# Optimization experiments

Measured on AMD Instinct MI355X. Metric: run time of the kernel, lower is better.

Reference implementation:

```python
import jax, jax.numpy as jnp
import numpy as np

E = 8            # num experts
D = 1024         # hidden size
F = 4096         # ffn hidden size
CAP_FACTOR = 2.0 # expert-choice capacity factor


def setup_inputs() -> dict:
    key = jax.random.key(0)
    ks = jax.random.split(key, 6)
    B, S = 8, 1024
    hidden_states = jax.random.normal(ks[0], (B, S, D), dtype=jnp.float32)
    Wg = jax.random.normal(ks[1], (D, E), dtype=jnp.float32) * (1.0 / np.sqrt(D))
    W1 = jax.random.normal(ks[2], (E, D, F), dtype=jnp.float32) * (1.0 / np.sqrt(D))
    b1 = jnp.zeros((E, F), dtype=jnp.float32)
    W2 = jax.random.normal(ks[3], (E, F, D), dtype=jnp.float32) * (1.0 / np.sqrt(F))
    b2 = jnp.zeros((E, D), dtype=jnp.float32)
    return {"hidden_states": hidden_states, "Wg": Wg, "W1": W1, "b1": b1,
            "W2": W2, "b2": b2}


def reference(hidden_states, Wg, W1, b1, W2, b2):
    B, S, d = hidden_states.shape
    T = B * S
    C = int(T * CAP_FACTOR / E)  # capacity per expert (static)

    x = hidden_states.reshape(T, d)                      # [T, D]
    gates = jax.nn.softmax(x @ Wg, axis=-1)              # [T, E] router probs

    # Expert-choice routing: each expert picks its top-C tokens.
    scores = gates.T                                     # [E, T]
    top_vals, idx = jax.lax.top_k(scores, C)             # [E, C]

    # Load-balancing aux loss (mean gate prob * fraction routed, per expert).
    frac_routed = jnp.zeros((T, E), gates.dtype).at[
        idx.reshape(-1), jnp.repeat(jnp.arange(E), C)].set(1.0).mean(axis=0)
    aux_loss = E * jnp.sum(gates.mean(axis=0) * frac_routed)

    # Grouped expert FFN on gathered tokens.
    xg = x[idx]                                          # [E, C, D]
    h = jax.nn.gelu(jnp.einsum('ecd,edf->ecf', xg, W1) + b1[:, None, :])
    yo = jnp.einsum('ecf,efd->ecd', h, W2) + b2[:, None, :]  # [E, C, D]

    # Weight by routing prob and scatter-add back to token positions.
    weighted = yo * top_vals[..., None]                  # [E, C, D]
    out = jnp.zeros((T, d), x.dtype).at[idx.reshape(-1)].add(
        weighted.reshape(-1, d))
    return out.reshape(B, S, d), aux_loss
```

## Files before the change

### kernel.cpp

```cpp
#include <hip/hip_runtime.h>
#include <hip/hip_bf16.h>

#define T_TOK 8192
#define E_EXP 8
#define D_HID 1024
#define F_FFN 4096
#define C_CAP 2048

typedef __attribute__((ext_vector_type(8))) short bf16x8;
typedef __attribute__((ext_vector_type(4))) float f32x4;

__device__ __forceinline__ void load_lds16(const void* g, void* l) {
    __builtin_amdgcn_global_load_lds(
        (const __attribute__((address_space(1))) unsigned int*)g,
        (__attribute__((address_space(3))) unsigned int*)l, 16, 0, 0);
}

__device__ __forceinline__ float gelu_fast(float v) {
    float z = v * (1.5957691216057308f + 0.07135481627f * v * v);
    return v / (1.0f + __expf(-z));
}

__global__ __launch_bounds__(256) void gating_kernel(
    const float* __restrict__ x, const float* __restrict__ Wg,
    float* __restrict__ gatesT, __hip_bfloat16* __restrict__ xbf,
    float* __restrict__ aux_out)
{
    const int token = blockIdx.x * 4 + (threadIdx.x >> 6);
    const int lane  = threadIdx.x & 63;
    if (token == 0 && lane == 0)
        aux_out[0] = (float)E_EXP * (float)C_CAP / (float)T_TOK;
    const float* xr = x + (size_t)token * D_HID;

    float acc[E_EXP];
#pragma unroll
    for (int e = 0; e < E_EXP; ++e) acc[e] = 0.0f;

#pragma unroll
    for (int it = 0; it < 4; ++it) {
        const int c4 = it * 64 + lane;
        float4 v = ((const float4*)xr)[c4];
        float vv[4] = {v.x, v.y, v.z, v.w};
        union { __hip_bfloat16 h[4]; short4 s; } u;
#pragma unroll
        for (int j = 0; j < 4; ++j) u.h[j] = __float2bfloat16(vv[j]);
        ((short4*)(xbf + (size_t)token * D_HID))[c4] = u.s;
        const float* wr0 = Wg + (size_t)c4 * 4 * E_EXP;
#pragma unroll
        for (int j = 0; j < 4; ++j)
#pragma unroll
            for (int e = 0; e < E_EXP; ++e) acc[e] += vv[j] * wr0[j * E_EXP + e];
    }
#pragma unroll
    for (int e = 0; e < E_EXP; ++e) {
        for (int off = 32; off; off >>= 1) acc[e] += __shfl_down(acc[e], off);
    }
    if (lane == 0) {
        float m = acc[0];
#pragma unroll
        for (int e = 1; e < E_EXP; ++e) m = fmaxf(m, acc[e]);
        float ex[E_EXP];
        float s = 0.0f;
#pragma unroll
        for (int e = 0; e < E_EXP; ++e) { ex[e] = expf(acc[e] - m); s += ex[e]; }
        float inv = 1.0f / s;
#pragma unroll
        for (int e = 0; e < E_EXP; ++e) gatesT[(size_t)e * T_TOK + token] = ex[e] * inv;
    }
}

__global__ __launch_bounds__(1024) void topk_kernel(
    const float* __restrict__ gatesT, int* __restrict__ topidx,
    float* __restrict__ topval, int* __restrict__ cnt, int* __restrict__ inv)
{
    __shared__ unsigned long long keys[T_TOK];
    __shared__ unsigned long long sel[C_CAP];
    __shared__ unsigned int hist[256];
    __shared__ unsigned int cum[256];
    __shared__ unsigned int bc_v, bc_r;
    __shared__ unsigned int selcnt;

    const int e   = blockIdx.x;
    const int tid = threadIdx.x;
    const float* row = gatesT + (size_t)e * T_TOK;

    for (int i = tid; i < T_TOK; i += 1024) {
        unsigned int b = __float_as_uint(row[i]);
        b = (b & 0x80000000u) ? ~b : (b | 0x80000000u);
        keys[i] = ((unsigned long long)b << 32) | (unsigned int)(T_TOK - 1 - i);
    }
    if (tid == 0) selcnt = 0;
    __syncthreads();

    unsigned long long prefix = 0ull, mask = 0ull;
    unsigned int rank = C_CAP;
    for (int byte = 7; byte >= 0; --byte) {
        if (tid < 256) hist[tid] = 0;
        __syncthreads();
        const int sh = byte * 8;
        for (int i = tid; i < T_TOK; i += 1024) {
            unsigned long long k = keys[i];
            if ((k & mask) == prefix)
                atomicAdd(&hist[(unsigned int)((k >> sh) & 255ull)], 1u);
        }
        __syncthreads();
        if (tid < 256) cum[tid] = hist[tid];
        __syncthreads();
        for (int off = 1; off < 256; off <<= 1) {
            unsigned int add = 0;
            if (tid < 256 && tid + off < 256) add = cum[tid + off];
            __syncthreads();
            if (tid < 256) cum[tid] += add;
            __syncthreads();
        }
        if (tid < 256) {
            unsigned int ge = cum[tid];
            unsigned int gt = (tid < 255) ? cum[tid + 1] : 0u;
            if (ge >= rank && gt < rank) { bc_v = (unsigned int)tid; bc_r = rank - gt; }
        }
        __syncthreads();
        prefix |= ((unsigned long long)bc_v) << sh;
        mask   |= (0xFFull << sh);
        rank = bc_r;
        __syncthreads();
    }
    const unsigned long long thr = prefix;

    for (int i = tid; i < T_TOK; i += 1024) {
        unsigned long long k = keys[i];
        if (k >= thr) sel[atomicAdd(&selcnt, 1u)] = k;
    }
    __syncthreads();

    for (int k = 2; k <= C_CAP; k <<= 1) {
        for (int j = k >> 1; j > 0; j >>= 1) {
            for (int i = tid; i < C_CAP; i += 1024) {
                int p = i ^ j;
                if (p > i) {
                    bool desc = ((i & k) == 0);
                    unsigned long long a = sel[i];
                    unsigned long long b = sel[p];
                    bool sw = desc ? (a < b) : (a > b);
                    if (sw) { sel[i] = b; sel[p] = a; }
                }
            }
            __syncthreads();
        }
    }

    for (int c = tid; c < C_CAP; c += 1024) {
        unsigned long long kk = sel[c];
        int idx = T_TOK - 1 - (int)(kk & 0xFFFFFFFFu);
        unsigned int b = (unsigned int)(kk >> 32);
        b = (b & 0x80000000u) ? (b & 0x7FFFFFFFu) : ~b;
        topidx[e * C_CAP + c] = idx;
        topval[e * C_CAP + c] = __uint_as_float(b);
        int slot = atomicAdd(&cnt[idx], 1);
        inv[idx * E_EXP + slot] = e * C_CAP + c;
    }
}

__global__ __launch_bounds__(256) void transpose_bf16_kernel(
    const float* __restrict__ in, __hip_bfloat16* __restrict__ out,
    int R, int Cn)
{
    __shared__ float tile[64][65];
    const int e = blockIdx.z;
    in  += (size_t)e * R * Cn;
    out += (size_t)e * R * Cn;
    const int c0 = blockIdx.x * 64, r0 = blockIdx.y * 64;
    const int tid = threadIdx.x;

    const int lr = tid >> 4, lc4 = (tid & 15) * 4;
#pragma unroll
    for (int it = 0; it < 4; ++it) {
        int r = lr + it * 16;
        float4 v = *(const float4*)(in + (size_t)(r0 + r) * Cn + c0 + lc4);
        tile[r][lc4 + 0] = v.x; tile[r][lc4 + 1] = v.y;
        tile[r][lc4 + 2] = v.z; tile[r][lc4 + 3] = v.w;
    }
    __syncthreads();

    const int ocb = tid >> 3, j0 = (tid & 7) * 8;
#pragma unroll
    for (int it = 0; it < 2; ++it) {
        int oc = ocb + it * 32;
        union { __hip_bfloat16 h[8]; uint4 v; } u;
#pragma unroll
        for (int j = 0; j < 8; ++j) u.h[j] = __float2bfloat16(tile[j0 + j][oc]);
        *(uint4*)(out + (size_t)(c0 + oc) * R + r0 + j0) = u.v;
    }
}


#define BARS do { __builtin_amdgcn_s_barrier(); __builtin_amdgcn_sched_barrier(0); } while (0)
#define WLG  do { asm volatile("s_waitcnt lgkmcnt(0)" ::: "memory"); __builtin_amdgcn_sched_barrier(0); } while (0)
#define VMC4 asm volatile("s_waitcnt vmcnt(4)" ::: "memory")
#define VMC0 asm volatile("s_waitcnt vmcnt(0)" ::: "memory")

#define G_STAGE_A(hh, s) do { int b_ = (((s) & 1) << 15) + ((hh) << 14) + (w << 10); \
    load_lds16(Abase + (size_t)(aog[hh][0] + (s) * 128), smem + b_); \
    load_lds16(Abase + (size_t)(aog[hh][1] + (s) * 128), smem + b_ + 8192); } while (0)
#define G_STAGE_B(hh, s) do { int b_ = 65536 + (((s) & 1) << 15) + ((hh) << 14) + (w << 10); \
    load_lds16(Bbase + (size_t)(bog[hh][0] + (s) * 128), smem + b_); \
    load_lds16(Bbase + (size_t)(bog[hh][1] + (s) * 128), smem + b_ + 8192); } while (0)

#define READ_A(mh) do { _Pragma("unroll") for (int mi = 0; mi < 4; ++mi) { \
    aF[mi][0] = *(const bf16x8*)(Ab + (arow + (mh) * 8192 + mi * 2048 + kc0)); \
    aF[mi][1] = *(const bf16x8*)(Ab + (arow + (mh) * 8192 + mi * 2048 + kc1)); } } while (0)
#define READ_B(nh, dst) do { _Pragma("unroll") for (int ni = 0; ni < 2; ++ni) { \
    dst[ni][0] = *(const bf16x8*)(Bb + (brow + (nh) * 4096 + ni * 2048 + kc0)); \
    dst[ni][1] = *(const bf16x8*)(Bb + (brow + (nh) * 4096 + ni * 2048 + kc1)); } } while (0)

#define QUAD(mh, nh, BF) do { \
    __builtin_amdgcn_s_setprio(1); \
    _Pragma("unroll") for (int mi = 0; mi < 4; ++mi) \
    _Pragma("unroll") for (int ni = 0; ni < 2; ++ni) { \
        acc[(mh)*4+mi][(nh)*2+ni] = __builtin_amdgcn_mfma_f32_16x16x32_bf16( \
            aF[mi][0], BF[ni][0], acc[(mh)*4+mi][(nh)*2+ni], 0, 0, 0); \
        acc[(mh)*4+mi][(nh)*2+ni] = __builtin_amdgcn_mfma_f32_16x16x32_bf16( \
            aF[mi][1], BF[ni][1], acc[(mh)*4+mi][(nh)*2+ni], 0, 0, 0); } \
    __builtin_amdgcn_s_setprio(0); } while (0)

#define GEMM_PROLOGUE() do { \
    G_STAGE_A(0, 0); G_STAGE_A(1, 0); G_STAGE_B(0, 0); G_STAGE_B(1, 0); \
    G_STAGE_B(0, 1); G_STAGE_B(1, 1); \
    VMC4; BARS; } while (0)

#define GEMM_TILE(t, NT) do { \
    const char* Ab = smem + (((t) & 1) << 15); \
    const char* Bb = smem + 65536 + (((t) & 1) << 15); \
     \
    READ_A(0); READ_B(0, bF0); \
    if ((t) + 1 < (NT)) G_STAGE_A(0, (t) + 1); \
    BARS; WLG; QUAD(0, 0, bF0); BARS; \
     \
    READ_B(1, bF1); \
    if ((t) + 1 < (NT)) G_STAGE_A(1, (t) + 1); \
    BARS; WLG; QUAD(0, 1, bF1); BARS; \
     \
    READ_A(1); \
    if ((t) + 2 < (NT)) G_STAGE_B(0, (t) + 2); \
    BARS; WLG; QUAD(1, 1, bF1); BARS; \
     \
    if ((t) + 2 < (NT)) G_STAGE_B(1, (t) + 2); \
    BARS; WLG; QUAD(1, 0, bF0); \
    if ((t) + 2 < (NT)) { VMC4; } else { VMC0; } \
    BARS; } while (0)

__global__ __launch_bounds__(512, 2) void gemm1_kernel(
    const __hip_bfloat16* __restrict__ xb,
    const __hip_bfloat16* __restrict__ W1t,
    const float* __restrict__ b1,
    const int* __restrict__ topidx,
    __hip_bfloat16* __restrict__ hbuf)
{
    __shared__ __align__(16) char smem[131072];
    const int tid = threadIdx.x;
    const int w = tid >> 6, lane = tid & 63;
    const int wr = w >> 2, wc = w & 3;
    const int fr = lane & 15, qlane = lane >> 4;

    const int bid = blockIdx.x;
    const int wg  = (bid & 7) * 128 + (bid >> 3);
    const int m0  = (wg & 7) * 256;
    const int n0  = ((wg >> 3) & 15) * 256;
    const int e   = wg >> 7;

    const char* Abase = (const char*)xb;
    const char* Bbase = (const char*)(W1t + (size_t)e * F_FFN * D_HID);

    const int cc = (tid & 7) ^ ((tid >> 3) & 7);
    int aog[2][2], bog[2][2];
#pragma unroll
    for (int hh = 0; hh < 2; ++hh)
#pragma unroll
        for (int j = 0; j < 2; ++j) {
            int r   = m0 + hh * 128 + j * 64 + (tid >> 3);
            int tok = topidx[e * C_CAP + r];
            aog[hh][j] = (tok * D_HID + cc * 8) * 2;
            int n = n0 + hh * 128 + j * 64 + (tid >> 3);
            bog[hh][j] = (n * D_HID + cc * 8) * 2;
        }

    const int arow = (wr * 128 + fr) * 128;
    const int brow = (wc * 64 + fr) * 128;
    const int kc0  = ((qlane)     ^ (lane & 7)) * 16;
    const int kc1  = ((4 + qlane) ^ (lane & 7)) * 16;

    bf16x8 aF[4][2], bF0[2][2], bF1[2][2];
    f32x4 acc[8][4];
#pragma unroll
    for (int mi = 0; mi < 8; ++mi)
#pragma unroll
        for (int ni = 0; ni < 4; ++ni) acc[mi][ni] = (f32x4){0.f, 0.f, 0.f, 0.f};

    GEMM_PROLOGUE();
    for (int t = 0; t < 16; ++t) GEMM_TILE(t, 16);

    const int q4 = qlane * 4;
    float b1v[4];
#pragma unroll
    for (int ni = 0; ni < 4; ++ni)
        b1v[ni] = b1[e * F_FFN + n0 + wc * 64 + ni * 16 + fr];
#pragma unroll
    for (int mi = 0; mi < 8; ++mi)
#pragma unroll
        for (int r = 0; r < 4; ++r) {
            const int row = wr * 128 + mi * 16 + q4 + r;
            char* rb = smem + row * 512;
            const int sw = (row & 7) << 4;
#pragma unroll
            for (int ni = 0; ni < 4; ++ni) {
                const int col2 = (wc * 64 + ni * 16 + fr) * 2;
                *(__hip_bfloat16*)(rb + (col2 ^ sw)) =
                    __float2bfloat16(gelu_fast(acc[mi][ni][r] + b1v[ni]));
            }
        }
    __syncthreads();
#pragma unroll
    for (int it = 0; it < 16; ++it) {
        const int row = it * 16 + w * 2 + (lane >> 5);
        const int cb  = (lane & 31) * 16;
        uint4 v = *(const uint4*)(smem + row * 512 + (cb ^ ((row & 7) << 4)));
        char* gp = (char*)(hbuf + ((size_t)e * C_CAP + m0 + row) * F_FFN + n0) + cb;
        *(uint4*)gp = v;
    }
}

__global__ __launch_bounds__(512, 2) void gemm2_kernel(
    const __hip_bfloat16* __restrict__ hbuf,
    const __hip_bfloat16* __restrict__ W2t,
    const float* __restrict__ b2,
    const float* __restrict__ topval,
    float* __restrict__ yo)
{
    __shared__ __align__(16) char smem[131072];
    const int tid = threadIdx.x;
    const int w = tid >> 6, lane = tid & 63;
    const int wr = w >> 2, wc = w & 3;
    const int fr = lane & 15, qlane = lane >> 4;

    const int bid = blockIdx.x;
    const int wg  = (bid & 7) * 32 + (bid >> 3);
    const int n0  = (wg & 3) * 256;
    const int m0  = ((wg >> 2) & 7) * 256;
    const int e   = wg >> 5;

    const char* Abase = (const char*)(hbuf + (size_t)e * C_CAP * F_FFN);
    const char* Bbase = (const char*)(W2t + (size_t)e * D_HID * F_FFN);

    const int cc = (tid & 7) ^ ((tid >> 3) & 7);
    int aog[2][2], bog[2][2];
#pragma unroll
    for (int hh = 0; hh < 2; ++hh)
#pragma unroll
        for (int j = 0; j < 2; ++j) {
            int r = m0 + hh * 128 + j * 64 + (tid >> 3);
            aog[hh][j] = (r * F_FFN + cc * 8) * 2;
            int n = n0 + hh * 128 + j * 64 + (tid >> 3);
            bog[hh][j] = (n * F_FFN + cc * 8) * 2;
        }

    const int arow = (wr * 128 + fr) * 128;
    const int brow = (wc * 64 + fr) * 128;
    const int kc0  = ((qlane)     ^ (lane & 7)) * 16;
    const int kc1  = ((4 + qlane) ^ (lane & 7)) * 16;

    bf16x8 aF[4][2], bF0[2][2], bF1[2][2];
    f32x4 acc[8][4];
#pragma unroll
    for (int mi = 0; mi < 8; ++mi)
#pragma unroll
        for (int ni = 0; ni < 4; ++ni) acc[mi][ni] = (f32x4){0.f, 0.f, 0.f, 0.f};

    GEMM_PROLOGUE();
    for (int t = 0; t < 64; ++t) GEMM_TILE(t, 64);

    const int q4 = qlane * 4;
    float b2v[4];
#pragma unroll
    for (int ni = 0; ni < 4; ++ni)
        b2v[ni] = b2[e * D_HID + n0 + wc * 64 + ni * 16 + fr];
#pragma unroll
    for (int mi = 0; mi < 8; ++mi)
#pragma unroll
        for (int r = 0; r < 4; ++r) {
            const int row = m0 + wr * 128 + mi * 16 + q4 + r;
            const float g = topval[e * C_CAP + row];
            float* orow = yo + ((size_t)e * C_CAP + row) * D_HID + n0 + wc * 64;
#pragma unroll
            for (int ni = 0; ni < 4; ++ni)
                orow[ni * 16 + fr] = (acc[mi][ni][r] + b2v[ni]) * g;
        }
}

__global__ __launch_bounds__(256) void combine_kernel(
    const float* __restrict__ yo, const int* __restrict__ cnt,
    const int* __restrict__ inv, float* __restrict__ out)
{
    const int t = blockIdx.x;
    const int n = cnt[t];
    const int c4 = threadIdx.x * 4;
    float4 a = {0.f, 0.f, 0.f, 0.f};
    for (int k = 0; k < n; ++k) {
        int ec = inv[t * E_EXP + k];
        float4 v = *(const float4*)(yo + (size_t)ec * D_HID + c4);
        a.x += v.x; a.y += v.y; a.z += v.z; a.w += v.w;
    }
    *(float4*)(out + (size_t)t * D_HID + c4) = a;
}

extern "C" void kernel_launch(void* const* d_in, const int* in_sizes, int n_in,
                              void* d_out, int out_size, void* d_ws, size_t ws_size,
                              hipStream_t stream) {
    const float* x  = (const float*)d_in[0];
    const float* Wg = (const float*)d_in[1];
    const float* W1 = (const float*)d_in[2];
    const float* b1 = (const float*)d_in[3];
    const float* W2 = (const float*)d_in[4];
    const float* b2 = (const float*)d_in[5];
    float* out = (float*)d_out;

    char* p = (char*)d_ws;
    float* gatesT = (float*)p;            p += (size_t)E_EXP * T_TOK * 4;
    int*   topidx = (int*)p;              p += (size_t)E_EXP * C_CAP * 4;
    float* topval = (float*)p;            p += (size_t)E_EXP * C_CAP * 4;
    int*   cnt    = (int*)p;              p += (size_t)T_TOK * 4;
    int*   inv    = (int*)p;              p += (size_t)T_TOK * E_EXP * 4;
    __hip_bfloat16* x_bf = (__hip_bfloat16*)p;  p += (size_t)T_TOK * D_HID * 2;
    __hip_bfloat16* W1t  = (__hip_bfloat16*)p;  p += (size_t)E_EXP * D_HID * F_FFN * 2;
    __hip_bfloat16* W2t  = (__hip_bfloat16*)p;  p += (size_t)E_EXP * D_HID * F_FFN * 2;
    __hip_bfloat16* hbuf = (__hip_bfloat16*)p;  p += (size_t)E_EXP * C_CAP * F_FFN * 2;
    float* yo = (float*)W1t;

    hipMemsetAsync(cnt, 0, (size_t)T_TOK * 4, stream);

    gating_kernel<<<T_TOK / 4, 256, 0, stream>>>(
        x, Wg, gatesT, x_bf, out + (size_t)T_TOK * D_HID);
    topk_kernel<<<E_EXP, 1024, 0, stream>>>(gatesT, topidx, topval, cnt, inv);

    {
        dim3 g(F_FFN / 64, D_HID / 64, E_EXP);
        transpose_bf16_kernel<<<g, 256, 0, stream>>>(W1, W1t, D_HID, F_FFN);
    }
    {
        dim3 g(D_HID / 64, F_FFN / 64, E_EXP);
        transpose_bf16_kernel<<<g, 256, 0, stream>>>(W2, W2t, F_FFN, D_HID);
    }

    gemm1_kernel<<<1024, 512, 0, stream>>>(x_bf, W1t, b1, topidx, hbuf);
    gemm2_kernel<<<256, 512, 0, stream>>>(hbuf, W2t, b2, topval, yo);
    combine_kernel<<<T_TOK, 256, 0, stream>>>(yo, cnt, inv, out);
}
```

Baseline: 700.2 us.

## Register-resident radix top-k without sort; gemm1 persistent over four N tiles

The top-k kernel now keeps its keys in registers instead of LDS. It replaces the 256-entry Hillis-Steele scan with a wavefront-shuffle suffix scan, and drops the bitonic sort, writing selected tokens in atomic order. gemm1 launches 256 blocks instead of 1024, and each block loops over four 256-column N tiles. This reuses the gathered A rows, precomputed addresses and pipeline setup across tiles, and writes GELU output straight to global memory instead of staging it through LDS. The risks are lower gemm1 occupancy, fewer blocks than CUs, uncoalesced bf16 stores, and a topidx order that is no longer sorted, which changes the row order of the results.

```diff
diff --git a/kernel.cpp b/kernel.cpp
--- a/kernel.cpp
+++ b/kernel.cpp
@@ -73,24 +73,24 @@
     const float* __restrict__ gatesT, int* __restrict__ topidx,
     float* __restrict__ topval, int* __restrict__ cnt, int* __restrict__ inv)
 {
-    __shared__ unsigned long long keys[T_TOK];
-    __shared__ unsigned long long sel[C_CAP];
     __shared__ unsigned int hist[256];
-    __shared__ unsigned int cum[256];
     __shared__ unsigned int bc_v, bc_r;
     __shared__ unsigned int selcnt;
 
-    const int e   = blockIdx.x;
-    const int tid = threadIdx.x;
+    const int e    = blockIdx.x;
+    const int tid  = threadIdx.x;
+    const int lane = tid & 63;
     const float* row = gatesT + (size_t)e * T_TOK;
 
-    for (int i = tid; i < T_TOK; i += 1024) {
+    unsigned long long kreg[8];
+#pragma unroll
+    for (int p = 0; p < 8; ++p) {
+        int i = tid + p * 1024;
         unsigned int b = __float_as_uint(row[i]);
         b = (b & 0x80000000u) ? ~b : (b | 0x80000000u);
-        keys[i] = ((unsigned long long)b << 32) | (unsigned int)(T_TOK - 1 - i);
+        kreg[p] = ((unsigned long long)b << 32) | (unsigned int)(T_TOK - 1 - i);
     }
     if (tid == 0) selcnt = 0;
-    __syncthreads();
 
     unsigned long long prefix = 0ull, mask = 0ull;
     unsigned int rank = C_CAP;
@@ -98,25 +98,31 @@
         if (tid < 256) hist[tid] = 0;
         __syncthreads();
         const int sh = byte * 8;
-        for (int i = tid; i < T_TOK; i += 1024) {
-            unsigned long long k = keys[i];
+#pragma unroll
+        for (int p = 0; p < 8; ++p) {
+            unsigned long long k = kreg[p];
             if ((k & mask) == prefix)
                 atomicAdd(&hist[(unsigned int)((k >> sh) & 255ull)], 1u);
         }
         __syncthreads();
-        if (tid < 256) cum[tid] = hist[tid];
-        __syncthreads();
-        for (int off = 1; off < 256; off <<= 1) {
-            unsigned int add = 0;
-            if (tid < 256 && tid + off < 256) add = cum[tid + off];
-            __syncthreads();
-            if (tid < 256) cum[tid] += add;
-            __syncthreads();
-        }
-        if (tid < 256) {
-            unsigned int ge = cum[tid];
-            unsigned int gt = (tid < 255) ? cum[tid + 1] : 0u;
-            if (ge >= rank && gt < rank) { bc_v = (unsigned int)tid; bc_r = rank - gt; }
+        if (tid < 64) {
+            unsigned int v0 = hist[tid * 4], v1 = hist[tid * 4 + 1];
+            unsigned int v2 = hist[tid * 4 + 2], v3 = hist[tid * 4 + 3];
+            unsigned int s3 = v3, s2 = v2 + s3, s1 = v1 + s2, s0 = v0 + s1;
+            unsigned int t = s0;
+#pragma unroll
+            for (int off = 1; off < 64; off <<= 1) {
+                unsigned int u = __shfl_down(t, off);
+                if (lane + off < 64) t += u;
+            }
+            const unsigned int suf = t - s0;
+            unsigned int ge[4] = {s0 + suf, s1 + suf, s2 + suf, s3 + suf};
+            unsigned int gt[4] = {s1 + suf, s2 + suf, s3 + suf, suf};
+#pragma unroll
+            for (int j = 0; j < 4; ++j)
+                if (ge[j] >= rank && gt[j] < rank) {
+                    bc_v = (unsigned int)(tid * 4 + j); bc_r = rank - gt[j];
+                }
         }
         __syncthreads();
         prefix |= ((unsigned long long)bc_v) << sh;
@@ -126,37 +132,19 @@
     }
     const unsigned long long thr = prefix;
 
-    for (int i = tid; i < T_TOK; i += 1024) {
-        unsigned long long k = keys[i];
-        if (k >= thr) sel[atomicAdd(&selcnt, 1u)] = k;
-    }
-    __syncthreads();
-
-    for (int k = 2; k <= C_CAP; k <<= 1) {
-        for (int j = k >> 1; j > 0; j >>= 1) {
-            for (int i = tid; i < C_CAP; i += 1024) {
-                int p = i ^ j;
-                if (p > i) {
-                    bool desc = ((i & k) == 0);
-                    unsigned long long a = sel[i];
-                    unsigned long long b = sel[p];
-                    bool sw = desc ? (a < b) : (a > b);
-                    if (sw) { sel[i] = b; sel[p] = a; }
-                }
-            }
-            __syncthreads();
-        }
-    }
-
-    for (int c = tid; c < C_CAP; c += 1024) {
-        unsigned long long kk = sel[c];
-        int idx = T_TOK - 1 - (int)(kk & 0xFFFFFFFFu);
-        unsigned int b = (unsigned int)(kk >> 32);
-        b = (b & 0x80000000u) ? (b & 0x7FFFFFFFu) : ~b;
-        topidx[e * C_CAP + c] = idx;
-        topval[e * C_CAP + c] = __uint_as_float(b);
-        int slot = atomicAdd(&cnt[idx], 1);
-        inv[idx * E_EXP + slot] = e * C_CAP + c;
+#pragma unroll
+    for (int p = 0; p < 8; ++p) {
+        unsigned long long k = kreg[p];
+        if (k >= thr) {
+            int c = (int)atomicAdd(&selcnt, 1u);
+            int idx = T_TOK - 1 - (int)(k & 0xFFFFFFFFull);
+            unsigned int b = (unsigned int)(k >> 32);
+            b = (b & 0x80000000u) ? (b & 0x7FFFFFFFu) : ~b;
+            topidx[e * C_CAP + c] = idx;
+            topval[e * C_CAP + c] = __uint_as_float(b);
+            int slot = atomicAdd(&cnt[idx], 1);
+            inv[idx * E_EXP + slot] = e * C_CAP + c;
+        }
     }
 }
 
@@ -198,12 +186,21 @@
 #define VMC4 asm volatile("s_waitcnt vmcnt(4)" ::: "memory")
 #define VMC0 asm volatile("s_waitcnt vmcnt(0)" ::: "memory")
 
-#define G_STAGE_A(hh, s) do { int b_ = (((s) & 1) << 15) + ((hh) << 14) + (w << 10); \
+#define STG2_A(hh, s) do { int b_ = (((s) & 1) << 15) + ((hh) << 14) + (w << 10); \
     load_lds16(Abase + (size_t)(aog[hh][0] + (s) * 128), smem + b_); \
     load_lds16(Abase + (size_t)(aog[hh][1] + (s) * 128), smem + b_ + 8192); } while (0)
-#define G_STAGE_B(hh, s) do { int b_ = 65536 + (((s) & 1) << 15) + ((hh) << 14) + (w << 10); \
+#define STG2_B(hh, s) do { int b_ = 65536 + (((s) & 1) << 15) + ((hh) << 14) + (w << 10); \
     load_lds16(Bbase + (size_t)(bog[hh][0] + (s) * 128), smem + b_); \
     load_lds16(Bbase + (size_t)(bog[hh][1] + (s) * 128), smem + b_ + 8192); } while (0)
+
+#define STG1_A(hh, s) do { int b_ = (((s) & 1) << 15) + ((hh) << 14) + (w << 10); \
+    int o_ = ((s) & 15) * 128; \
+    load_lds16(Abase + (size_t)(aog[hh][0] + o_), smem + b_); \
+    load_lds16(Abase + (size_t)(aog[hh][1] + o_), smem + b_ + 8192); } while (0)
+#define STG1_B(hh, s) do { int b_ = 65536 + (((s) & 1) << 15) + ((hh) << 14) + (w << 10); \
+    int o_ = ((s) >> 4) * 524288 + ((s) & 15) * 128; \
+    load_lds16(Bbase + (size_t)(bog[hh][0] + o_), smem + b_); \
+    load_lds16(Bbase + (size_t)(bog[hh][1] + o_), smem + b_ + 8192); } while (0)
 
 #define READ_A(mh) do { _Pragma("unroll") for (int mi = 0; mi < 4; ++mi) { \
     aF[mi][0] = *(const bf16x8*)(Ab + (arow + (mh) * 8192 + mi * 2048 + kc0)); \
@@ -222,28 +219,28 @@
             aF[mi][1], BF[ni][1], acc[(mh)*4+mi][(nh)*2+ni], 0, 0, 0); } \
     __builtin_amdgcn_s_setprio(0); } while (0)
 
-#define GEMM_PROLOGUE() do { \
-    G_STAGE_A(0, 0); G_STAGE_A(1, 0); G_STAGE_B(0, 0); G_STAGE_B(1, 0); \
-    G_STAGE_B(0, 1); G_STAGE_B(1, 1); \
+#define GEMM_PROLOGUE_G(SA, SB) do { \
+    SA(0, 0); SA(1, 0); SB(0, 0); SB(1, 0); \
+    SB(0, 1); SB(1, 1); \
     VMC4; BARS; } while (0)
 
-#define GEMM_TILE(t, NT) do { \
+#define GEMM_TILE_G(t, NT, SA, SB) do { \
     const char* Ab = smem + (((t) & 1) << 15); \
     const char* Bb = smem + 65536 + (((t) & 1) << 15); \
      \
     READ_A(0); READ_B(0, bF0); \
-    if ((t) + 1 < (NT)) G_STAGE_A(0, (t) + 1); \
+    if ((t) + 1 < (NT)) SA(0, (t) + 1); \
     BARS; WLG; QUAD(0, 0, bF0); BARS; \
      \
     READ_B(1, bF1); \
-    if ((t) + 1 < (NT)) G_STAGE_A(1, (t) + 1); \
+    if ((t) + 1 < (NT)) SA(1, (t) + 1); \
     BARS; WLG; QUAD(0, 1, bF1); BARS; \
      \
     READ_A(1); \
-    if ((t) + 2 < (NT)) G_STAGE_B(0, (t) + 2); \
+    if ((t) + 2 < (NT)) SB(0, (t) + 2); \
     BARS; WLG; QUAD(1, 1, bF1); BARS; \
      \
-    if ((t) + 2 < (NT)) G_STAGE_B(1, (t) + 2); \
+    if ((t) + 2 < (NT)) SB(1, (t) + 2); \
     BARS; WLG; QUAD(1, 0, bF0); \
     if ((t) + 2 < (NT)) { VMC4; } else { VMC0; } \
     BARS; } while (0)
@@ -262,10 +259,11 @@
     const int fr = lane & 15, qlane = lane >> 4;
 
     const int bid = blockIdx.x;
-    const int wg  = (bid & 7) * 128 + (bid >> 3);
-    const int m0  = (wg & 7) * 256;
-    const int n0  = ((wg >> 3) & 15) * 256;
-    const int e   = wg >> 7;
+    const int wg  = (bid & 7) * 32 + (bid >> 3);
+    const int nc  = wg & 3;
+    const int m0  = ((wg >> 2) & 7) * 256;
+    const int e   = wg >> 5;
+    const int nc0 = nc * 1024;
 
     const char* Abase = (const char*)xb;
     const char* Bbase = (const char*)(W1t + (size_t)e * F_FFN * D_HID);
@@ -279,9 +277,16 @@
             int r   = m0 + hh * 128 + j * 64 + (tid >> 3);
             int tok = topidx[e * C_CAP + r];
             aog[hh][j] = (tok * D_HID + cc * 8) * 2;
-            int n = n0 + hh * 128 + j * 64 + (tid >> 3);
+            int n = nc0 + hh * 128 + j * 64 + (tid >> 3);
             bog[hh][j] = (n * D_HID + cc * 8) * 2;
         }
+
+    float b1all[4][4];
+#pragma unroll
+    for (int p = 0; p < 4; ++p)
+#pragma unroll
+        for (int ni = 0; ni < 4; ++ni)
+            b1all[p][ni] = b1[e * F_FFN + nc0 + p * 256 + wc * 64 + ni * 16 + fr];
 
     const int arow = (wr * 128 + fr) * 128;
     const int brow = (wc * 64 + fr) * 128;
@@ -295,36 +300,30 @@
 #pragma unroll
         for (int ni = 0; ni < 4; ++ni) acc[mi][ni] = (f32x4){0.f, 0.f, 0.f, 0.f};
 
-    GEMM_PROLOGUE();
-    for (int t = 0; t < 16; ++t) GEMM_TILE(t, 16);
-
+    GEMM_PROLOGUE_G(STG1_A, STG1_B);
     const int q4 = qlane * 4;
-    float b1v[4];
-#pragma unroll
-    for (int ni = 0; ni < 4; ++ni)
-        b1v[ni] = b1[e * F_FFN + n0 + wc * 64 + ni * 16 + fr];
-#pragma unroll
-    for (int mi = 0; mi < 8; ++mi)
-#pragma unroll
-        for (int r = 0; r < 4; ++r) {
-            const int row = wr * 128 + mi * 16 + q4 + r;
-            char* rb = smem + row * 512;
-            const int sw = (row & 7) << 4;
-#pragma unroll
-            for (int ni = 0; ni < 4; ++ni) {
-                const int col2 = (wc * 64 + ni * 16 + fr) * 2;
-                *(__hip_bfloat16*)(rb + (col2 ^ sw)) =
-                    __float2bfloat16(gelu_fast(acc[mi][ni][r] + b1v[ni]));
+#pragma unroll 1
+    for (int p = 0; p < 4; ++p) {
+#pragma unroll 2
+        for (int tl = 0; tl < 16; ++tl) {
+            const int t = p * 16 + tl;
+            GEMM_TILE_G(t, 64, STG1_A, STG1_B);
+        }
+        const int n0p = nc0 + p * 256;
+#pragma unroll
+        for (int mi = 0; mi < 8; ++mi) {
+#pragma unroll
+            for (int r = 0; r < 4; ++r) {
+                size_t row = (size_t)e * C_CAP + m0 + wr * 128 + mi * 16 + q4 + r;
+                __hip_bfloat16* orow = hbuf + row * F_FFN + n0p + wc * 64;
+#pragma unroll
+                for (int ni = 0; ni < 4; ++ni)
+                    orow[ni * 16 + fr] =
+                        __float2bfloat16(gelu_fast(acc[mi][ni][r] + b1all[p][ni]));
             }
-        }
-    __syncthreads();
-#pragma unroll
-    for (int it = 0; it < 16; ++it) {
-        const int row = it * 16 + w * 2 + (lane >> 5);
-        const int cb  = (lane & 31) * 16;
-        uint4 v = *(const uint4*)(smem + row * 512 + (cb ^ ((row & 7) << 4)));
-        char* gp = (char*)(hbuf + ((size_t)e * C_CAP + m0 + row) * F_FFN + n0) + cb;
-        *(uint4*)gp = v;
+#pragma unroll
+            for (int ni = 0; ni < 4; ++ni) acc[mi][ni] = (f32x4){0.f, 0.f, 0.f, 0.f};
+        }
     }
 }
 
@@ -374,8 +373,9 @@
 #pragma unroll
         for (int ni = 0; ni < 4; ++ni) acc[mi][ni] = (f32x4){0.f, 0.f, 0.f, 0.f};
 
-    GEMM_PROLOGUE();
-    for (int t = 0; t < 64; ++t) GEMM_TILE(t, 64);
+    GEMM_PROLOGUE_G(STG2_A, STG2_B);
+#pragma unroll 2
+    for (int t = 0; t < 64; ++t) GEMM_TILE_G(t, 64, STG2_A, STG2_B);
 
     const int q4 = qlane * 4;
     float b2v[4];
@@ -383,7 +383,7 @@
     for (int ni = 0; ni < 4; ++ni)
         b2v[ni] = b2[e * D_HID + n0 + wc * 64 + ni * 16 + fr];
 #pragma unroll
-    for (int mi = 0; mi < 8; ++mi)
+    for (int mi = 0; mi < 8; ++mi) {
 #pragma unroll
         for (int r = 0; r < 4; ++r) {
             const int row = m0 + wr * 128 + mi * 16 + q4 + r;
@@ -393,6 +393,7 @@
             for (int ni = 0; ni < 4; ++ni)
                 orow[ni * 16 + fr] = (acc[mi][ni][r] + b2v[ni]) * g;
         }
+    }
 }
 
 __global__ __launch_bounds__(256) void combine_kernel(
@@ -449,7 +450,7 @@
         transpose_bf16_kernel<<<g, 256, 0, stream>>>(W2, W2t, F_FFN, D_HID);
     }
 
-    gemm1_kernel<<<1024, 512, 0, stream>>>(x_bf, W1t, b1, topidx, hbuf);
+    gemm1_kernel<<<256, 512, 0, stream>>>(x_bf, W1t, b1, topidx, hbuf);
     gemm2_kernel<<<256, 512, 0, stream>>>(hbuf, W2t, b2, topval, yo);
     combine_kernel<<<T_TOK, 256, 0, stream>>>(yo, cnt, inv, out);
 }
```

Result: faster. 664.7 us (-5.1%).
